# Optimization experiments

Measured on AMD Instinct MI355X. Metric: run time of the kernel, lower is better.

The kernel has to match this reference:

```python
import jax, jax.numpy as jnp
import numpy as np

B = 64; N_PER = 128; N = B * N_PER          # 8192 nodes
E = 32768                                    # edges
X_DIM = 64; EDGE_DIM = 16; D = 512
RING_SIZE = 6; RINGS_PER = 8; R = B * RINGS_PER  # 512 rings
NH_RING = 2; NH_MOL = 4; DFF = 4 * D
GAT_LAYERS = 6; NEG_SLOPE = 0.2


def _ln(x, g, b, eps=1e-5):
    mu = jnp.mean(x, axis=-1, keepdims=True)
    var = jnp.mean((x - mu) ** 2, axis=-1, keepdims=True)
    return (x - mu) * jax.lax.rsqrt(var + eps) * g + b


def _seg_softmax(s, seg, n):
    m = jax.ops.segment_max(s, seg, num_segments=n)
    e = jnp.exp(s - m[seg])
    z = jax.ops.segment_sum(e, seg, num_segments=n)
    return e / z[seg]


def _mha(x, w, b, nh):
    Bq, S, Dm = x.shape
    dh = Dm // nh
    q = (x @ w[0] + b[0]).reshape(Bq, S, nh, dh)
    k = (x @ w[1] + b[1]).reshape(Bq, S, nh, dh)
    v = (x @ w[2] + b[2]).reshape(Bq, S, nh, dh)
    att = jax.nn.softmax(jnp.einsum('bqhd,bkhd->bhqk', q, k) / np.float32(np.sqrt(dh)), axis=-1)
    o = jnp.einsum('bhqk,bkhd->bqhd', att, v).reshape(Bq, S, Dm)
    return o @ w[3] + b[3]


def _encoder(x, aw, ab, w1, b1, w2, b2, lns, nh):
    # post-LN transformer encoder block (1 layer)
    y = _ln(x + _mha(x, aw, ab, nh), lns[0, 0], lns[0, 1])
    h = jnp.maximum(y @ w1 + b1, 0.0) @ w2 + b2
    return _ln(y + h, lns[1, 0], lns[1, 1])


def setup_inputs() -> dict:
    key = jax.random.key(0)
    ks = jax.random.split(key, 24)
    f32 = jnp.float32
    def p(i, shape, s=0.02):
        return jax.random.normal(ks[i], shape, f32) * s
    ln2 = jnp.stack([jnp.stack([jnp.ones((D,), f32), jnp.zeros((D,), f32)])] * 2)  # [2,2,D]
    return {
        'x': jax.random.normal(ks[0], (N, X_DIM), f32),
        'edge_attr': jax.random.normal(ks[1], (E, EDGE_DIM), f32),
        'edge_index': jax.random.randint(ks[2], (2, E), 0, N, jnp.int32),
        'rings_node_index': jax.random.randint(ks[3], (R * RING_SIZE,), 0, N, jnp.int32),
        'rings_node_nums': jnp.full((R,), RING_SIZE, jnp.int32),
        'mol_rings_nums': jnp.full((B,), RINGS_PER, jnp.int32),
        'batch': jnp.repeat(jnp.arange(B, dtype=jnp.int32), N_PER),
        'ptr': jnp.arange(B + 1, dtype=jnp.int32) * N_PER,
        'x_proj_w': p(4, (X_DIM, D)), 'x_proj_b': jnp.zeros((D,), f32),
        'e_proj_w': p(5, (EDGE_DIM, D)), 'e_proj_b': jnp.zeros((D,), f32),
        'gat_wl': p(6, (GAT_LAYERS, D, D)), 'gat_bl': jnp.zeros((GAT_LAYERS, D), f32),
        'gat_wr': p(7, (GAT_LAYERS, D, D)), 'gat_br': jnp.zeros((GAT_LAYERS, D), f32),
        'gat_we': p(8, (GAT_LAYERS, D, D)),
        'gat_att': p(9, (GAT_LAYERS, D)),
        'gat_bias': jnp.zeros((GAT_LAYERS, D), f32),
        'gat_ln': jnp.stack([jnp.ones((GAT_LAYERS - 1, D), f32), jnp.zeros((GAT_LAYERS - 1, D), f32)], axis=1),
        'ring_attn_w': p(10, (4, D, D)), 'ring_attn_b': jnp.zeros((4, D), f32),
        'ring_w1': p(11, (D, DFF)), 'ring_b1': jnp.zeros((DFF,), f32),
        'ring_w2': p(12, (DFF, D)), 'ring_b2': jnp.zeros((D,), f32),
        'ring_ln': ln2,
        'mol_attn_w': p(13, (4, D, D)), 'mol_attn_b': jnp.zeros((4, D), f32),
        'mol_w1': p(14, (D, DFF)), 'mol_b1': jnp.zeros((DFF,), f32),
        'mol_w2': p(15, (DFF, D)), 'mol_b2': jnp.zeros((D,), f32),
        'mol_ln': ln2,
        'cls_tok': p(16, (1, D), 1.0), 'ring_tok': p(17, (1, D), 1.0), 'end_tok': p(18, (1, D), 1.0),
    }


def reference(x, edge_attr, edge_index, rings_node_index, rings_node_nums,
              mol_rings_nums, batch, ptr,
              x_proj_w, x_proj_b, e_proj_w, e_proj_b,
              gat_wl, gat_bl, gat_wr, gat_br, gat_we, gat_att, gat_bias, gat_ln,
              ring_attn_w, ring_attn_b, ring_w1, ring_b1, ring_w2, ring_b2, ring_ln,
              mol_attn_w, mol_attn_b, mol_w1, mol_b1, mol_w2, mol_b2, mol_ln,
              cls_tok, ring_tok, end_tok):
    # 1) input projections
    h = x @ x_proj_w + x_proj_b                   # [N, D]
    e = edge_attr @ e_proj_w + e_proj_b           # [E, D]
    src, dst = edge_index[0], edge_index[1]
    # self-loops with mean incoming edge attr (PyG fill_value='mean')
    deg = jax.ops.segment_sum(jnp.ones((E,), h.dtype), dst, num_segments=N)
    loop_e = jax.ops.segment_sum(e, dst, num_segments=N) / jnp.maximum(deg, 1.0)[:, None]
    loops = jnp.arange(N, dtype=src.dtype)
    src_e = jnp.concatenate([src, loops])
    dst_e = jnp.concatenate([dst, loops])
    e_all = jnp.concatenate([e, loop_e], axis=0)  # [E+N, D]
    # 2) 6-layer GATv2 (heads=1), LayerNorm+ReLU between layers
    for l in range(GAT_LAYERS):
        xl = h @ gat_wl[l] + gat_bl[l]
        xr = h @ gat_wr[l] + gat_br[l]
        m = jax.nn.leaky_relu(xl[src_e] + xr[dst_e] + e_all @ gat_we[l], NEG_SLOPE)
        a = _seg_softmax(m @ gat_att[l], dst_e, N)
        out = jax.ops.segment_sum(a[:, None] * xl[src_e], dst_e, num_segments=N) + gat_bias[l]
        if l < GAT_LAYERS - 1:
            out = jnp.maximum(_ln(out, gat_ln[l, 0], gat_ln[l, 1]), 0.0)
        h = out
    # 3) rings attention: gather ring atoms, encode, per-channel abs-argmax gather
    t = h[rings_node_index].reshape(R, RING_SIZE, D)
    t = _encoder(t, ring_attn_w, ring_attn_b, ring_w1, ring_b1, ring_w2, ring_b2, ring_ln, NH_RING)
    idx = jnp.argmax(jnp.abs(t), axis=1)                         # [R, D]
    rings_vec = jnp.take_along_axis(t, idx[:, None, :], axis=1)[:, 0, :]  # [R, D]
    # 4) split/pad per molecule (uniform sizes -> reshape) and assemble sequence
    X = h.reshape(B, N_PER, D)
    Xr = rings_vec.reshape(B, RINGS_PER, D)
    seq = jnp.concatenate([
        jnp.broadcast_to(cls_tok[None], (B, 1, D)), X,
        jnp.broadcast_to(ring_tok[None], (B, 1, D)), Xr,
        jnp.broadcast_to(end_tok[None], (B, 1, D))], axis=1)     # [B, 139, D]
    seq = _encoder(seq, mol_attn_w, mol_attn_b, mol_w1, mol_b1, mol_w2, mol_b2, mol_ln, NH_MOL)
    not_padded_X = jnp.ones((B, N_PER), dtype=bool)
    not_padded_Xr = jnp.ones((B, RINGS_PER), dtype=bool)
    return seq, not_padded_X, not_padded_Xr
```

## Files before the change

kernel.cpp:

```cpp
#include <hip/hip_runtime.h>
#include <math.h>


#define DEV __device__ __forceinline__

constexpr int NN   = 8192;
constexpr int EE   = 32768;
constexpr int ENL  = EE + NN;
constexpr int D    = 512;
constexpr int RGS  = 512;
constexpr int RS   = 6;
constexpr int BMOL = 64;
constexpr int SEQS = 139;
constexpr int NSEQ = BMOL * SEQS;
constexpr int MHAT = 8960;
constexpr int DFF  = 2048;

typedef short bf8 __attribute__((ext_vector_type(8)));
typedef float f32x4 __attribute__((ext_vector_type(4)));
typedef _Float16 half2_t __attribute__((ext_vector_type(2)));
typedef _Float16 half8_t __attribute__((ext_vector_type(8)));

#ifdef __has_builtin
#if __has_builtin(__builtin_amdgcn_fdot2)
#define HAS_FDOT2 1
#endif
#endif
#ifndef HAS_FDOT2
#define HAS_FDOT2 0
#endif

DEV float wsum(float v) {
    for (int o = 32; o > 0; o >>= 1) v += __shfl_xor(v, o, 64);
    return v;
}
DEV float wmax(float v) {
    for (int o = 32; o > 0; o >>= 1) v = fmaxf(v, __shfl_xor(v, o, 64));
    return v;
}
DEV unsigned short f2bf(float x) {
    unsigned u = __float_as_uint(x);
    u += 0x7FFFu + ((u >> 16) & 1u);
    return (unsigned short)(u >> 16);
}
DEV float bf2f(unsigned short h) { return __uint_as_float((unsigned)h << 16); }

DEV float dot8(half8_t a, half8_t b, float acc) {
#if HAS_FDOT2
    acc = __builtin_amdgcn_fdot2(__builtin_shufflevector(a, a, 0, 1),
                                 __builtin_shufflevector(b, b, 0, 1), acc, false);
    acc = __builtin_amdgcn_fdot2(__builtin_shufflevector(a, a, 2, 3),
                                 __builtin_shufflevector(b, b, 2, 3), acc, false);
    acc = __builtin_amdgcn_fdot2(__builtin_shufflevector(a, a, 4, 5),
                                 __builtin_shufflevector(b, b, 4, 5), acc, false);
    acc = __builtin_amdgcn_fdot2(__builtin_shufflevector(a, a, 6, 7),
                                 __builtin_shufflevector(b, b, 6, 7), acc, false);
#else
#pragma unroll
    for (int i = 0; i < 8; ++i) acc += (float)a[i] * (float)b[i];
#endif
    return acc;
}

struct GB {
    const float* A;
    const float* B0; const float* B1; const float* B2;
    const float* bias0; const float* bias1; const float* bias2;
    float* C0; float* C1; float* C2;
    int M, N, K, flags, kparts, ksz;
    long long cstride;
};

__global__ __launch_bounds__(256) void gemm_f32b(GB g) {
    __shared__ float As[16][132];
    __shared__ float Bs[16][128];
    const int z = blockIdx.z;
    const int bb = z / g.kparts, kp = z % g.kparts;
    const float* B = bb == 0 ? g.B0 : (bb == 1 ? g.B1 : g.B2);
    const float* bias = bb == 0 ? g.bias0 : (bb == 1 ? g.bias1 : g.bias2);
    float* C = (bb == 0 ? g.C0 : (bb == 1 ? g.C1 : g.C2)) + (size_t)kp * g.cstride;
    const int M = g.M, N = g.N;

    const int tid = threadIdx.x;
    const int wv = tid >> 6, ln = tid & 63;
    const int mg = ((ln >> 3) & 7) | ((wv & 1) << 3);
    const int ng = (ln & 7) | ((wv >> 1) << 3);
    const int m0 = blockIdx.x * 128, n0 = blockIdx.y * 128;

    const int a_row = tid >> 2;
    const int a_kg  = tid & 3;
    const int b_row = tid >> 5;
    const int b_cg  = tid & 31;

    float acc[8][8] = {};
    const int kbeg = kp * g.ksz, kend = kbeg + g.ksz;
    for (int k0 = kbeg; k0 < kend; k0 += 16) {
#pragma unroll
        for (int i = 0; i < 2; ++i) {
            int r = a_row + i * 64;
            int gr = m0 + r; if (gr >= M) gr = M - 1;
            float4 av = *(const float4*)&g.A[(size_t)gr * g.K + k0 + a_kg * 4];
            As[a_kg * 4 + 0][r] = av.x;
            As[a_kg * 4 + 1][r] = av.y;
            As[a_kg * 4 + 2][r] = av.z;
            As[a_kg * 4 + 3][r] = av.w;
        }
#pragma unroll
        for (int i = 0; i < 2; ++i) {
            int r = b_row + i * 8;
            float4 bv = *(const float4*)&B[(size_t)(k0 + r) * N + n0 + b_cg * 4];
            *(float4*)&Bs[r][b_cg * 4] = bv;
        }
        __syncthreads();
#pragma unroll
        for (int k = 0; k < 16; ++k) {
            float a0[8], b0[8];
            *(float4*)&a0[0] = *(const float4*)&As[k][mg * 8];
            *(float4*)&a0[4] = *(const float4*)&As[k][mg * 8 + 4];
            *(float4*)&b0[0] = *(const float4*)&Bs[k][ng * 8];
            *(float4*)&b0[4] = *(const float4*)&Bs[k][ng * 8 + 4];
#pragma unroll
            for (int i = 0; i < 8; ++i)
#pragma unroll
                for (int j = 0; j < 8; ++j) acc[i][j] += a0[i] * b0[j];
        }
        __syncthreads();
    }
#pragma unroll
    for (int i = 0; i < 8; ++i) {
        int gr = m0 + mg * 8 + i;
        if (gr >= M) break;
        float* cp = &C[(size_t)gr * N + n0 + ng * 8];
        float o[8];
#pragma unroll
        for (int j = 0; j < 8; ++j) o[j] = acc[i][j];
        if ((g.flags & 1) && g.kparts == 1) {
            const float* bp = bias + n0 + ng * 8;
#pragma unroll
            for (int j = 0; j < 8; ++j) o[j] += bp[j];
        }
        if (g.flags & 2) {
#pragma unroll
            for (int j = 0; j < 8; ++j) o[j] = fmaxf(o[j], 0.f);
        }
        *(float4*)&cp[0] = make_float4(o[0], o[1], o[2], o[3]);
        *(float4*)&cp[4] = make_float4(o[4], o[5], o[6], o[7]);
    }
}

__global__ __launch_bounds__(256) void gemm_split3(
    const unsigned short* __restrict__ Ah, const unsigned short* __restrict__ Al,
    const unsigned short* __restrict__ Bh, const unsigned short* __restrict__ Bl,
    const float* __restrict__ bias, float* __restrict__ C,
    unsigned short* __restrict__ Ch, unsigned short* __restrict__ Cl,
    int N, int K, int flags, long long bstride, long long cstride, int biasstride)
{
    __shared__ unsigned short sA[2][128][40];
    __shared__ unsigned short sB[2][128][40];
    const int z = blockIdx.z;
    Bh += (size_t)z * bstride; Bl += (size_t)z * bstride;
    if (bias) bias += (size_t)z * biasstride;
    if (C) C += (size_t)z * cstride;
    const int tid = threadIdx.x;
    const int wv = tid >> 6, lane = tid & 63;
    const int m0 = blockIdx.x * 128, n0 = blockIdx.y * 128;
    const int srow = tid >> 2, sc8 = (tid & 3) * 8;
    const int mw = (wv & 1) * 64, nw = (wv >> 1) * 64;
    const int fr = lane & 15, fq = lane >> 4;
    const int ko = fq * 8;

    f32x4 acc[4][4];
    f32x4 zero = {0.f, 0.f, 0.f, 0.f};
#pragma unroll
    for (int i = 0; i < 4; ++i)
#pragma unroll
        for (int j = 0; j < 4; ++j) acc[i][j] = zero;

    for (int k0 = 0; k0 < K; k0 += 32) {
#pragma unroll
        for (int h = 0; h < 2; ++h) {
            int r = srow + h * 64;
            *(bf8*)&sA[0][r][sc8] = *(const bf8*)&Ah[(size_t)(m0 + r) * K + k0 + sc8];
            *(bf8*)&sA[1][r][sc8] = *(const bf8*)&Al[(size_t)(m0 + r) * K + k0 + sc8];
            *(bf8*)&sB[0][r][sc8] = *(const bf8*)&Bh[(size_t)(n0 + r) * K + k0 + sc8];
            *(bf8*)&sB[1][r][sc8] = *(const bf8*)&Bl[(size_t)(n0 + r) * K + k0 + sc8];
        }
        __syncthreads();
        bf8 ah[4], al[4], bh[4], bl[4];
#pragma unroll
        for (int t = 0; t < 4; ++t) {
            ah[t] = *(const bf8*)&sA[0][mw + t * 16 + fr][ko];
            al[t] = *(const bf8*)&sA[1][mw + t * 16 + fr][ko];
            bh[t] = *(const bf8*)&sB[0][nw + t * 16 + fr][ko];
            bl[t] = *(const bf8*)&sB[1][nw + t * 16 + fr][ko];
        }
#pragma unroll
        for (int i = 0; i < 4; ++i)
#pragma unroll
            for (int j = 0; j < 4; ++j) {
                acc[i][j] = __builtin_amdgcn_mfma_f32_16x16x32_bf16(ah[i], bh[j], acc[i][j], 0, 0, 0);
                acc[i][j] = __builtin_amdgcn_mfma_f32_16x16x32_bf16(ah[i], bl[j], acc[i][j], 0, 0, 0);
                acc[i][j] = __builtin_amdgcn_mfma_f32_16x16x32_bf16(al[i], bh[j], acc[i][j], 0, 0, 0);
            }
        __syncthreads();
    }
#pragma unroll
    for (int i = 0; i < 4; ++i)
#pragma unroll
        for (int j = 0; j < 4; ++j) {
            int col = n0 + nw + j * 16 + fr;
#pragma unroll
            for (int r = 0; r < 4; ++r) {
                int row = m0 + mw + i * 16 + fq * 4 + r;
                float o = acc[i][j][r];
                if (flags & 1) o += bias[col];
                if (flags & 2) o = fmaxf(o, 0.f);
                size_t idx = (size_t)row * N + col;
                if (flags & 4) {
                    unsigned short hb_ = f2bf(o);
                    Ch[idx] = hb_;
                    Cl[idx] = f2bf(o - bf2f(hb_));
                } else {
                    C[idx] = o;
                }
            }
        }
}

__global__ void asplit4(const float* __restrict__ src, unsigned short* __restrict__ hh,
                        unsigned short* __restrict__ ll, int n4) {
    int i = blockIdx.x * 256 + threadIdx.x;
    if (i >= n4) return;
    float4 v = ((const float4*)src)[i];
    ushort4 h, l;
    h.x = f2bf(v.x); l.x = f2bf(v.x - bf2f(h.x));
    h.y = f2bf(v.y); l.y = f2bf(v.y - bf2f(h.y));
    h.z = f2bf(v.z); l.z = f2bf(v.z - bf2f(h.z));
    h.w = f2bf(v.w); l.w = f2bf(v.w - bf2f(h.w));
    ((ushort4*)hh)[i] = h;
    ((ushort4*)ll)[i] = l;
}

__global__ void wsplitT(const float* __restrict__ w, unsigned short* __restrict__ bh,
                        unsigned short* __restrict__ bl, int K, int N) {
    int i = blockIdx.x * 256 + threadIdx.x;
    if (i >= K * N) return;
    int k = i / N, n = i - k * N;
    float x = w[i];
    unsigned short h = f2bf(x);
    unsigned short l = f2bf(x - bf2f(h));
    bh[(size_t)n * K + k] = h;
    bl[(size_t)n * K + k] = l;
}

__global__ __launch_bounds__(256) void ln_rows(
    const float* __restrict__ x, const float* __restrict__ res,
    const float* __restrict__ bias, const float* __restrict__ g,
    const float* __restrict__ be, float* __restrict__ out, int rows, int flags,
    int parts)
{
    int r = blockIdx.x * 4 + (threadIdx.x >> 6);
    if (r >= rows) return;
    int lane = threadIdx.x & 63;
    size_t base = (size_t)r * D;
    size_t pstride = (size_t)rows * D;
    float v[8];
#pragma unroll
    for (int i = 0; i < 8; ++i) {
        int d = lane + i * 64;
        float t = x[base + d];
        for (int p = 1; p < parts; ++p) t += x[p * pstride + base + d];
        if (res)  t += res[base + d];
        if (bias) t += bias[d];
        v[i] = t;
    }
    if (flags & 2) {
        float s = 0;
#pragma unroll
        for (int i = 0; i < 8; ++i) s += v[i];
        float mu = wsum(s) * (1.f / 512.f);
        float q = 0;
#pragma unroll
        for (int i = 0; i < 8; ++i) { float d0 = v[i] - mu; q += d0 * d0; }
        float inv = rsqrtf(wsum(q) * (1.f / 512.f) + 1e-5f);
#pragma unroll
        for (int i = 0; i < 8; ++i) {
            int d = lane + i * 64;
            float o = (v[i] - mu) * inv * g[d] + be[d];
            if (flags & 1) o = fmaxf(o, 0.f);
            out[base + d] = o;
        }
    } else {
#pragma unroll
        for (int i = 0; i < 8; ++i) {
            int d = lane + i * 64;
            float o = v[i];
            if (flags & 1) o = fmaxf(o, 0.f);
            out[base + d] = o;
        }
    }
}

__global__ void fill_f32(float* p, float v, int n) {
    int i = blockIdx.x * 256 + threadIdx.x;
    if (i < n) p[i] = v;
}

__global__ void deg_int(const int* __restrict__ ei, int* __restrict__ degi) {
    int e = blockIdx.x * 256 + threadIdx.x;
    if (e >= EE) return;
    atomicAdd(&degi[ei[EE + e]], 1);
}

__global__ __launch_bounds__(256) void scan_deg(const int* __restrict__ degi,
                                                int* __restrict__ off) {
    __shared__ int ps[256];
    int tid = threadIdx.x;
    int base = tid * 32;
    int loc[32];
    int s = 0;
#pragma unroll
    for (int i = 0; i < 32; ++i) { loc[i] = s; s += degi[base + i]; }
    ps[tid] = s;
    __syncthreads();
    for (int o = 1; o < 256; o <<= 1) {
        int v = (tid >= o) ? ps[tid - o] : 0;
        __syncthreads();
        ps[tid] += v;
        __syncthreads();
    }
    int pre = (tid == 0) ? 0 : ps[tid - 1];
#pragma unroll
    for (int i = 0; i < 32; ++i) off[base + i] = pre + loc[i];
    if (tid == 255) off[8192] = ps[255];
}

__global__ void csr_fill(const int* __restrict__ ei, int* __restrict__ cnt,
                         const int* __restrict__ off, int* __restrict__ adj) {
    int e = blockIdx.x * 256 + threadIdx.x;
    if (e >= EE) return;
    int dn = ei[EE + e];
    int p = atomicAdd(&cnt[dn], 1);
    adj[off[dn] + p] = e;
}

__global__ void eagg_acc(const float* __restrict__ eattr, const int* __restrict__ ei,
                         float* __restrict__ agg) {
    int id = blockIdx.x * 256 + threadIdx.x;
    if (id >= EE * 16) return;
    int e = id >> 4, c = id & 15;
    atomicAdd(&agg[(size_t)ei[EE + e] * 16 + c], eattr[id]);
}

__global__ void ein_build(const float* __restrict__ eattr, const float* __restrict__ agg,
                          const int* __restrict__ degi, float* __restrict__ ein) {
    int r = blockIdx.x * 256 + threadIdx.x;
    if (r >= ENL) return;
    float* o = &ein[(size_t)r * 17];
    if (r < EE) {
        const float* a = &eattr[(size_t)r * 16];
#pragma unroll
        for (int k = 0; k < 16; ++k) o[k] = a[k];
        o[16] = 1.f;
    } else {
        int n = r - EE;
        int dg = degi[n];
        float inv = 1.f / (float)(dg > 1 ? dg : 1);
        const float* a = &agg[(size_t)n * 16];
#pragma unroll
        for (int k = 0; k < 16; ++k) o[k] = a[k] * inv;
        o[16] = dg > 0 ? 1.f : 0.f;
    }
}

__global__ __launch_bounds__(256) void we17_build(
    const float* __restrict__ epw, const float* __restrict__ epb,
    const float* __restrict__ we_all, float* __restrict__ we17_all) {
    int j = blockIdx.x * 256 + threadIdx.x;
    int kk = blockIdx.y, l = blockIdx.z;
    const float* we = we_all + (size_t)l * D * D;
    float* we17 = we17_all + (size_t)l * 17 * D;
    float acc[17];
#pragma unroll
    for (int i = 0; i < 17; ++i) acc[i] = 0.f;
    for (int k = kk * 128; k < kk * 128 + 128; ++k) {
        float wkj = we[(size_t)k * 512 + j];
#pragma unroll
        for (int i = 0; i < 16; ++i) acc[i] += epw[(size_t)i * 512 + k] * wkj;
        acc[16] += epb[k] * wkj;
    }
#pragma unroll
    for (int i = 0; i < 17; ++i) atomicAdd(&we17[(size_t)i * 512 + j], acc[i]);
}

__global__ __launch_bounds__(256) void gat_node(
    const float* __restrict__ xl, const float* __restrict__ xr,
    const float* __restrict__ ein, const float* __restrict__ we17,
    const int* __restrict__ off, const int* __restrict__ adj,
    const int* __restrict__ ei, const float* __restrict__ att,
    float* __restrict__ out)
{
    __shared__ float we[17][512];
    __shared__ float sc[4][88];
    int tid = threadIdx.x;
    for (int i = tid; i < 17 * 512; i += 256) we[i >> 9][i & 511] = we17[i];
    __syncthreads();
    int wv = tid >> 6, lane = tid & 63;
    int n = blockIdx.x * 4 + wv;
    float xr8[8], att8[8];
#pragma unroll
    for (int i = 0; i < 8; ++i) {
        int d = lane + i * 64;
        xr8[i] = xr[(size_t)n * D + d];
        att8[i] = att[d];
    }
    int o0 = off[n];
    int deg = off[n + 1] - o0;
    if (deg > 80) deg = 80;
    for (int j = 0; j <= deg; ++j) {
        int er, s;
        if (j < deg) { int e = adj[o0 + j]; er = e; s = ei[e]; }
        else         { er = EE + n; s = n; }
        const float* ep = &ein[(size_t)er * 17];
        float e17[17];
#pragma unroll
        for (int k = 0; k < 17; ++k) e17[k] = ep[k];
        float a = 0;
#pragma unroll
        for (int i = 0; i < 8; ++i) {
            int d = lane + i * 64;
            float m = xl[(size_t)s * D + d] + xr8[i];
#pragma unroll
            for (int k = 0; k < 17; ++k) m += e17[k] * we[k][d];
            m = m > 0.f ? m : 0.2f * m;
            a += att8[i] * m;
        }
        a = wsum(a);
        if (lane == 0) sc[wv][j] = a;
    }
    __syncthreads();
    float mx = -1e30f;
    for (int j = 0; j <= deg; ++j) mx = fmaxf(mx, sc[wv][j]);
    float z = 0;
    for (int j = 0; j <= deg; ++j) z += expf(sc[wv][j] - mx);
    float acc[8] = {};
    for (int j = 0; j <= deg; ++j) {
        int s = (j < deg) ? ei[adj[o0 + j]] : n;
        float w = expf(sc[wv][j] - mx);
#pragma unroll
        for (int i = 0; i < 8; ++i) acc[i] += w * xl[(size_t)s * D + lane + i * 64];
    }
    float inv = 1.f / z;
#pragma unroll
    for (int i = 0; i < 8; ++i) out[(size_t)n * D + lane + i * 64] = acc[i] * inv;
}

__global__ void gather_rows(const float* __restrict__ src, const int* __restrict__ idx,
                            float* __restrict__ dst, int nrows) {
    int i = blockIdx.x * 256 + threadIdx.x;
    int r = i >> 9;
    if (r >= nrows) return;
    dst[i] = src[(size_t)idx[r] * D + (i & 511)];
}

__global__ __launch_bounds__(256) void ring_attn(
    const float* __restrict__ q, const float* __restrict__ k,
    const float* __restrict__ v, float* __restrict__ o)
{
    int rh = blockIdx.x, r = rh >> 1, hh = rh & 1;
    __shared__ float qs[RS * 256], ks[RS * 256], vs[RS * 256];
    __shared__ float scs[36], pr[36];
    int tid = threadIdx.x;
    size_t base = (size_t)r * RS * D + hh * 256;
    for (int i = tid; i < RS * 256; i += 256) {
        int si = i >> 8, d = i & 255;
        size_t g = base + (size_t)si * D + d;
        qs[i] = q[g]; ks[i] = k[g]; vs[i] = v[g];
    }
    __syncthreads();
    if (tid < 36) {
        int i = tid / 6, j = tid % 6;
        float a = 0;
        for (int d = 0; d < 256; ++d) a += qs[i * 256 + d] * ks[j * 256 + d];
        scs[tid] = a * (1.f / 16.f);
    }
    __syncthreads();
    if (tid < 6) {
        float mx = -1e30f;
        for (int j = 0; j < 6; ++j) mx = fmaxf(mx, scs[tid * 6 + j]);
        float p[6], s = 0;
        for (int j = 0; j < 6; ++j) { p[j] = expf(scs[tid * 6 + j] - mx); s += p[j]; }
        for (int j = 0; j < 6; ++j) pr[tid * 6 + j] = p[j] / s;
    }
    __syncthreads();
    for (int i = tid; i < RS * 256; i += 256) {
        int si = i >> 8, d = i & 255;
        float a = 0;
        for (int j = 0; j < 6; ++j) a += pr[si * 6 + j] * vs[j * 256 + d];
        o[base + (size_t)si * D + d] = a;
    }
}

constexpr int ATT_K_H  = SEQS * 128;
constexpr int ATT_V_ROW = 152;
constexpr int ATT_V_H  = 128 * ATT_V_ROW;
constexpr int ATT_PS_ROW = 144;
constexpr int ATT_PS_H = 8 * ATT_PS_ROW;
constexpr int ATT_SMEM = (ATT_K_H + ATT_V_H + ATT_PS_H) * 2 + 8 * 64 * 4;

__global__ __launch_bounds__(256) void mol_attn3(
    const float* __restrict__ q, const float* __restrict__ k,
    const float* __restrict__ v, float* __restrict__ o)
{
    extern __shared__ char smem[];
    _Float16* Ksh = (_Float16*)smem;
    _Float16* Vt  = Ksh + ATT_K_H;
    _Float16* ps  = Vt + ATT_V_H;
    half2_t*  qs  = (half2_t*)(ps + ATT_PS_H);
    const int tid = threadIdx.x, wv = tid >> 6, lane = tid & 63;
    const int b = blockIdx.x >> 2, hh = blockIdx.x & 3;
    const size_t hb = (size_t)b * SEQS * D + hh * 128;

    for (int i = tid; i < SEQS * 32; i += 256) {
        int j = i >> 5, d4 = i & 31;
        float4 kv = *(const float4*)&k[hb + (size_t)j * D + d4 * 4];
        int off = j * 128 + (((d4 >> 1) ^ (j & 7)) << 3) + ((d4 & 1) << 2);
        *(half2_t*)(Ksh + off)     = half2_t{(_Float16)kv.x, (_Float16)kv.y};
        *(half2_t*)(Ksh + off + 2) = half2_t{(_Float16)kv.z, (_Float16)kv.w};
    }
    for (int i = tid; i < SEQS * 32; i += 256) {
        int j = i >> 5, d4 = i & 31;
        float4 vv = *(const float4*)&v[hb + (size_t)j * D + d4 * 4];
        Vt[(d4 * 4 + 0) * ATT_V_ROW + j] = (_Float16)vv.x;
        Vt[(d4 * 4 + 1) * ATT_V_ROW + j] = (_Float16)vv.y;
        Vt[(d4 * 4 + 2) * ATT_V_ROW + j] = (_Float16)vv.z;
        Vt[(d4 * 4 + 3) * ATT_V_ROW + j] = (_Float16)vv.w;
    }
    for (int i = tid; i < 128 * 5; i += 256) {
        int d = i / 5, jt = SEQS + i % 5;
        Vt[d * ATT_V_ROW + jt] = (_Float16)0.f;
    }
    __syncthreads();

    const float scale = 0.08838834764831845f;
    for (int t = 0; t < 18; ++t) {
        int p = wv + 4 * t;
        if (p >= 70) continue;
        int q0 = 2 * p, q1 = 2 * p + 1;
        bool h1 = q1 < SEQS;
        {
            float2 f0 = *(const float2*)&q[hb + (size_t)q0 * D + lane * 2];
            qs[(wv * 2 + 0) * 64 + lane] = half2_t{(_Float16)f0.x, (_Float16)f0.y};
            if (h1) {
                float2 f1 = *(const float2*)&q[hb + (size_t)q1 * D + lane * 2];
                qs[(wv * 2 + 1) * 64 + lane] = half2_t{(_Float16)f1.x, (_Float16)f1.y};
            }
        }
        float s0[3], s1[3];
#pragma unroll
        for (int jj = 0; jj < 3; ++jj) { s0[jj] = -1e30f; s1[jj] = -1e30f; }
#pragma unroll
        for (int jj = 0; jj < 3; ++jj) {
            int j = lane + jj * 64;
            if (j < SEQS) {
                float a0 = 0, a1 = 0;
                const int jb = j * 128, jx = j & 7;
#pragma unroll
                for (int c = 0; c < 16; ++c) {
                    half8_t kk = *(const half8_t*)(Ksh + jb + ((c ^ jx) << 3));
                    half8_t q0v = *(const half8_t*)(qs + (wv * 2 + 0) * 64 + c * 4);
                    a0 = dot8(kk, q0v, a0);
                    if (h1) {
                        half8_t q1v = *(const half8_t*)(qs + (wv * 2 + 1) * 64 + c * 4);
                        a1 = dot8(kk, q1v, a1);
                    }
                }
                s0[jj] = a0 * scale; s1[jj] = a1 * scale;
            }
        }
        {
            float m0 = wmax(fmaxf(fmaxf(s0[0], s0[1]), s0[2]));
            float z0 = 0; float e0[3];
#pragma unroll
            for (int jj = 0; jj < 3; ++jj) {
                int j = lane + jj * 64;
                e0[jj] = (j < SEQS) ? expf(s0[jj] - m0) : 0.f;
                z0 += e0[jj];
            }
            z0 = wsum(z0); float inv0 = 1.f / z0;
#pragma unroll
            for (int jj = 0; jj < 3; ++jj) {
                int j = lane + jj * 64;
                if (j < ATT_PS_ROW) ps[(wv * 2 + 0) * ATT_PS_ROW + j] = (_Float16)(e0[jj] * inv0);
            }
        }
        if (h1) {
            float m1 = wmax(fmaxf(fmaxf(s1[0], s1[1]), s1[2]));
            float z1 = 0; float e1[3];
#pragma unroll
            for (int jj = 0; jj < 3; ++jj) {
                int j = lane + jj * 64;
                e1[jj] = (j < SEQS) ? expf(s1[jj] - m1) : 0.f;
                z1 += e1[jj];
            }
            z1 = wsum(z1); float inv1 = 1.f / z1;
#pragma unroll
            for (int jj = 0; jj < 3; ++jj) {
                int j = lane + jj * 64;
                if (j < ATT_PS_ROW) ps[(wv * 2 + 1) * ATT_PS_ROW + j] = (_Float16)(e1[jj] * inv1);
            }
        }
        float o00 = 0, o01 = 0, o10 = 0, o11 = 0;
#pragma unroll
        for (int c8 = 0; c8 < 18; ++c8) {
            half8_t va = *(const half8_t*)(Vt + lane * ATT_V_ROW + c8 * 8);
            half8_t vb = *(const half8_t*)(Vt + (lane + 64) * ATT_V_ROW + c8 * 8);
            half8_t p0 = *(const half8_t*)(ps + (wv * 2 + 0) * ATT_PS_ROW + c8 * 8);
            o00 = dot8(va, p0, o00);
            o01 = dot8(vb, p0, o01);
            if (h1) {
                half8_t p1 = *(const half8_t*)(ps + (wv * 2 + 1) * ATT_PS_ROW + c8 * 8);
                o10 = dot8(va, p1, o10);
                o11 = dot8(vb, p1, o11);
            }
        }
        o[hb + (size_t)q0 * D + lane]      = o00;
        o[hb + (size_t)q0 * D + lane + 64] = o01;
        if (h1) {
            o[hb + (size_t)q1 * D + lane]      = o10;
            o[hb + (size_t)q1 * D + lane + 64] = o11;
        }
    }
}

__global__ void ring_pick(const float* __restrict__ t, float* __restrict__ rv) {
    int i = blockIdx.x * 256 + threadIdx.x;
    if (i >= RGS * D) return;
    int r = i >> 9, d = i & 511;
    const float* p = &t[(size_t)r * RS * D + d];
    float best = p[0], ba = fabsf(best);
#pragma unroll
    for (int s = 1; s < RS; ++s) {
        float x = p[(size_t)s * D];
        float ax = fabsf(x);
        if (ax > ba) { ba = ax; best = x; }
    }
    rv[i] = best;
}

__global__ void assemble(const float* __restrict__ h, const float* __restrict__ rv,
                         const float* __restrict__ cls, const float* __restrict__ ringt,
                         const float* __restrict__ endt, float* __restrict__ seq) {
    int i = blockIdx.x * 256 + threadIdx.x;
    if (i >= NSEQ * D) return;
    int row = i >> 9, d = i & 511;
    int b = row / SEQS, p = row % SEQS;
    float val;
    if (p == 0)        val = cls[d];
    else if (p <= 128) val = h[((size_t)b * 128 + (p - 1)) * D + d];
    else if (p == 129) val = ringt[d];
    else if (p <= 137) val = rv[((size_t)b * 8 + (p - 130)) * D + d];
    else               val = endt[d];
    seq[i] = val;
}

extern "C" void kernel_launch(void* const* d_in, const int* in_sizes, int n_in,
                              void* d_out, int out_size, void* d_ws, size_t ws_size,
                              hipStream_t stream) {
    (void)in_sizes; (void)n_in; (void)out_size; (void)ws_size;

    const float* x          = (const float*)d_in[0];
    const float* edge_attr  = (const float*)d_in[1];
    const int*   ei         = (const int*)  d_in[2];
    const int*   rings_idx  = (const int*)  d_in[3];
    const float* x_proj_w   = (const float*)d_in[8];
    const float* x_proj_b   = (const float*)d_in[9];
    const float* e_proj_w   = (const float*)d_in[10];
    const float* e_proj_b   = (const float*)d_in[11];
    const float* gat_wl     = (const float*)d_in[12];
    const float* gat_bl     = (const float*)d_in[13];
    const float* gat_wr     = (const float*)d_in[14];
    const float* gat_br     = (const float*)d_in[15];
    const float* gat_we     = (const float*)d_in[16];
    const float* gat_att    = (const float*)d_in[17];
    const float* gat_bias   = (const float*)d_in[18];
    const float* gat_ln     = (const float*)d_in[19];
    const float* ring_attn_w= (const float*)d_in[20];
    const float* ring_attn_b= (const float*)d_in[21];
    const float* ring_w1    = (const float*)d_in[22];
    const float* ring_b1    = (const float*)d_in[23];
    const float* ring_w2    = (const float*)d_in[24];
    const float* ring_b2    = (const float*)d_in[25];
    const float* ring_ln    = (const float*)d_in[26];
    const float* mol_attn_w = (const float*)d_in[27];
    const float* mol_attn_b = (const float*)d_in[28];
    const float* mol_w1     = (const float*)d_in[29];
    const float* mol_b1     = (const float*)d_in[30];
    const float* mol_w2     = (const float*)d_in[31];
    const float* mol_b2     = (const float*)d_in[32];
    const float* mol_ln     = (const float*)d_in[33];
    const float* cls_tok    = (const float*)d_in[34];
    const float* ring_tok   = (const float*)d_in[35];
    const float* end_tok    = (const float*)d_in[36];

    constexpr size_t MB = 1024 * 1024;
    char* wsb = (char*)d_ws;
#define WSF(off) ((float*)(wsb + (size_t)(off)))
#define WSI(off) ((int*)(wsb + (size_t)(off)))
#define WSU(off) ((unsigned short*)(wsb + (size_t)(off)))

    float* H    = WSF(0);
    float* XL   = WSF(16 * MB);
    float* XR   = WSF(32 * MB);
    float* HN   = WSF(48 * MB);
    float* EIN  = WSF(64 * MB);
    float* WE17 = WSF(67 * MB);
    float* AGG  = WSF(68 * MB);
    int*   DEGI = WSI(68 * MB + 512 * 1024);
    int*   OFF  = WSI(68 * MB + 576 * 1024);
    int*   CNT  = WSI(68 * MB + 640 * 1024);
    int*   ADJ  = WSI(68 * MB + 704 * 1024);
    float* RVEC = WSF(70 * MB);

    float* T    = WSF(71 * MB);
    float* RQ   = WSF(77 * MB);
    float* RK   = WSF(83 * MB);
    float* RV   = WSF(89 * MB);
    float* RO   = WSF(95 * MB);
    float* OP   = WSF(101 * MB);
    float* RY   = WSF(113 * MB);
    float* RFF  = WSF(119 * MB);
    float* W2P  = WSF(143 * MB);
    float* RT2  = WSF(167 * MB);

    float* SEQ  = WSF(71 * MB);
    float* MQKV = WSF(89 * MB);
    float* MO   = WSF(142 * MB);
    unsigned short* ACTh = WSU(161 * MB);
    unsigned short* ACTl = WSU(170 * MB);
    unsigned short* WQKVh = WSU(179 * MB);
    unsigned short* WQKVl = WSU(181 * MB);
    unsigned short* WOh  = WSU(183 * MB);
    unsigned short* WOl  = WSU(183 * MB + 512 * 1024);
    unsigned short* W1h  = WSU(184 * MB);
    unsigned short* W1l  = WSU(186 * MB);
    unsigned short* W2h  = WSU(188 * MB);
    unsigned short* W2l  = WSU(190 * MB);
    float* MTMP = WSF(89 * MB);
    float* MY   = WSF(107 * MB);
    unsigned short* MFFh = WSU(125 * MB);
    unsigned short* MFFl = WSU(16 * MB);
    float* MT2  = WSF(71 * MB);

    dim3 blk(256);
    auto gemm1 = [&](const float* A, const float* B, const float* bias, float* C,
                     int M, int Nc, int K, int flags) {
        GB g{A, B, nullptr, nullptr, bias, nullptr, nullptr, C, nullptr, nullptr,
             M, Nc, K, flags, 1, K, 0};
        gemm_f32b<<<dim3(M / 128, Nc / 128, 1), blk, 0, stream>>>(g);
    };

    hipMemsetAsync(DEGI, 0, NN * 4, stream);
    hipMemsetAsync(CNT, 0, NN * 4, stream);
    hipMemsetAsync(AGG, 0, (size_t)NN * 16 * 4, stream);
    hipMemsetAsync(WE17, 0, (size_t)6 * 17 * D * 4, stream);
    deg_int<<<EE / 256, blk, 0, stream>>>(ei, DEGI);
    scan_deg<<<1, blk, 0, stream>>>(DEGI, OFF);
    csr_fill<<<EE / 256, blk, 0, stream>>>(ei, CNT, OFF, ADJ);
    eagg_acc<<<EE * 16 / 256, blk, 0, stream>>>(edge_attr, ei, AGG);
    ein_build<<<ENL / 256, blk, 0, stream>>>(edge_attr, AGG, DEGI, EIN);
    we17_build<<<dim3(2, 4, 6), blk, 0, stream>>>(e_proj_w, e_proj_b, gat_we, WE17);

    gemm1(x, x_proj_w, x_proj_b, H, NN, D, 64, 1);

    for (int l = 0; l < 6; ++l) {
        GB g{H, gat_wl + (size_t)l * D * D, gat_wr + (size_t)l * D * D, nullptr,
             gat_bl + l * D, gat_br + l * D, nullptr,
             XL, XR, nullptr, NN, D, D, 1, 1, D, 0};
        gemm_f32b<<<dim3(NN / 128, D / 128, 2), blk, 0, stream>>>(g);
        gat_node<<<NN / 4, blk, 0, stream>>>(XL, XR, EIN, WE17 + (size_t)l * 17 * D,
                                             OFF, ADJ, ei, gat_att + l * D, HN);
        if (l < 5) {
            ln_rows<<<NN / 4, blk, 0, stream>>>(HN, nullptr, gat_bias + l * D,
                gat_ln + (size_t)l * 2 * D, gat_ln + (size_t)l * 2 * D + D, H, NN, 3, 1);
        } else {
            ln_rows<<<NN / 4, blk, 0, stream>>>(HN, nullptr, gat_bias + l * D,
                nullptr, nullptr, H, NN, 0, 1);
        }
    }

    const int RROWS = RGS * RS;
    gather_rows<<<RROWS * D / 256, blk, 0, stream>>>(H, rings_idx, T, RROWS);
    {
        GB g{T, ring_attn_w + 0 * D * D, ring_attn_w + 1 * D * D, ring_attn_w + 2 * D * D,
             ring_attn_b + 0 * D, ring_attn_b + 1 * D, ring_attn_b + 2 * D,
             RQ, RK, RV, RROWS, D, D, 1, 1, D, 0};
        gemm_f32b<<<dim3(RROWS / 128, D / 128, 3), blk, 0, stream>>>(g);
    }
    ring_attn<<<RGS * 2, blk, 0, stream>>>(RQ, RK, RV, RO);
    {
        GB g{RO, ring_attn_w + 3 * D * D, nullptr, nullptr, nullptr, nullptr, nullptr,
             OP, nullptr, nullptr, RROWS, D, D, 0, 2, 256, (long long)RROWS * D};
        gemm_f32b<<<dim3(RROWS / 128, D / 128, 2), blk, 0, stream>>>(g);
    }
    ln_rows<<<RROWS / 4, blk, 0, stream>>>(OP, T, ring_attn_b + 3 * D,
                                           ring_ln, ring_ln + D, RY, RROWS, 2, 2);
    gemm1(RY, ring_w1, ring_b1, RFF, RROWS, DFF, D, 3);
    {
        GB g{RFF, ring_w2, nullptr, nullptr, nullptr, nullptr, nullptr,
             W2P, nullptr, nullptr, RROWS, D, DFF, 0, 4, 512, (long long)RROWS * D};
        gemm_f32b<<<dim3(RROWS / 128, D / 128, 4), blk, 0, stream>>>(g);
    }
    ln_rows<<<RROWS / 4, blk, 0, stream>>>(W2P, RY, ring_b2,
                                           ring_ln + 2 * D, ring_ln + 3 * D, RT2, RROWS, 2, 4);
    ring_pick<<<RGS * D / 256, blk, 0, stream>>>(RT2, RVEC);

    assemble<<<(NSEQ * D) / 256, blk, 0, stream>>>(H, RVEC, cls_tok, ring_tok, end_tok, SEQ);
    for (int z = 0; z < 3; ++z)
        wsplitT<<<(D * D + 255) / 256, blk, 0, stream>>>(
            mol_attn_w + (size_t)z * D * D, WQKVh + (size_t)z * D * D, WQKVl + (size_t)z * D * D, D, D);
    wsplitT<<<(D * D + 255) / 256, blk, 0, stream>>>(mol_attn_w + 3 * (size_t)D * D, WOh, WOl, D, D);
    wsplitT<<<(D * DFF + 255) / 256, blk, 0, stream>>>(mol_w1, W1h, W1l, D, DFF);
    wsplitT<<<(DFF * D + 255) / 256, blk, 0, stream>>>(mol_w2, W2h, W2l, DFF, D);

    const int N4_512 = MHAT * D / 4;
    float* MQ = MQKV;
    float* MK = MQKV + (size_t)MHAT * D;
    float* MV = MQKV + 2 * (size_t)MHAT * D;
    asplit4<<<(N4_512 + 255) / 256, blk, 0, stream>>>(SEQ, ACTh, ACTl, N4_512);
    gemm_split3<<<dim3(MHAT / 128, D / 128, 3), blk, 0, stream>>>(
        ACTh, ACTl, WQKVh, WQKVl, mol_attn_b, MQKV, nullptr, nullptr,
        D, D, 1, (long long)D * D, (long long)MHAT * D, D);

    hipFuncSetAttribute(reinterpret_cast<const void*>(mol_attn3),
                        hipFuncAttributeMaxDynamicSharedMemorySize, ATT_SMEM);
    mol_attn3<<<BMOL * 4, blk, ATT_SMEM, stream>>>(MQ, MK, MV, MO);

    asplit4<<<(N4_512 + 255) / 256, blk, 0, stream>>>(MO, ACTh, ACTl, N4_512);
    gemm_split3<<<dim3(MHAT / 128, D / 128, 1), blk, 0, stream>>>(
        ACTh, ACTl, WOh, WOl, mol_attn_b + 3 * D, MTMP, nullptr, nullptr, D, D, 1, 0, 0, 0);
    ln_rows<<<(NSEQ + 3) / 4, blk, 0, stream>>>(MTMP, SEQ, nullptr,
                                                mol_ln, mol_ln + D, MY, NSEQ, 2, 1);
    asplit4<<<(N4_512 + 255) / 256, blk, 0, stream>>>(MY, ACTh, ACTl, N4_512);
    gemm_split3<<<dim3(MHAT / 128, DFF / 128, 1), blk, 0, stream>>>(
        ACTh, ACTl, W1h, W1l, mol_b1, nullptr, MFFh, MFFl, DFF, D, 1 | 2 | 4, 0, 0, 0);
    gemm_split3<<<dim3(MHAT / 128, D / 128, 1), blk, 0, stream>>>(
        MFFh, MFFl, W2h, W2l, mol_b2, MT2, nullptr, nullptr, D, DFF, 1, 0, 0, 0);

    float* outf = (float*)d_out;
    ln_rows<<<(NSEQ + 3) / 4, blk, 0, stream>>>(MT2, MY, nullptr,
                                                mol_ln + 2 * D, mol_ln + 3 * D, outf, NSEQ, 2, 1);
    fill_f32<<<(BMOL * 128 + BMOL * 8 + 255) / 256, blk, 0, stream>>>(
        outf + (size_t)NSEQ * D, 1.0f, BMOL * 128 + BMOL * 8);
}
```

Baseline: 2.318 ms.

## Split-K GEMMs with atomic accumulation, swap grid axes, fuse QKV into one GEMM

The fp32 GEMM kernel gains an atomic-accumulate mode: GAT and ring projections run split-K into zeroed buffers, with the bias added only by the first K-part. ReLU is moved from the W1 epilogue into the W2 A-load so split-K stays correct. Grid axes are swapped so N tiles vary fastest, aiming for better reuse of A rows in cache. The molecule QKV projection becomes one GEMM with N=1536 and interleaved output rows read by attention through a row stride. In exchange it adds memsets and atomic traffic, and it assumes the split-3 weights are laid out contiguously so a single N=1536 GEMM is valid.

Result: slower. 5.386 ms (+132.4%).

```diff
diff --git a/kernel.cpp b/kernel.cpp
--- a/kernel.cpp
+++ b/kernel.cpp
@@ -75,17 +75,18 @@
     __shared__ float As[16][132];
     __shared__ float Bs[16][128];
     const int z = blockIdx.z;
-    const int bb = z / g.kparts, kp = z % g.kparts;
+    const int bb = z / g.kparts, kp = z - bb * g.kparts;
     const float* B = bb == 0 ? g.B0 : (bb == 1 ? g.B1 : g.B2);
     const float* bias = bb == 0 ? g.bias0 : (bb == 1 ? g.bias1 : g.bias2);
-    float* C = (bb == 0 ? g.C0 : (bb == 1 ? g.C1 : g.C2)) + (size_t)kp * g.cstride;
+    float* C = (bb == 0 ? g.C0 : (bb == 1 ? g.C1 : g.C2));
+    if (!(g.flags & 4)) C += (size_t)kp * g.cstride;
     const int M = g.M, N = g.N;
 
     const int tid = threadIdx.x;
     const int wv = tid >> 6, ln = tid & 63;
     const int mg = ((ln >> 3) & 7) | ((wv & 1) << 3);
     const int ng = (ln & 7) | ((wv >> 1) << 3);
-    const int m0 = blockIdx.x * 128, n0 = blockIdx.y * 128;
+    const int m0 = blockIdx.y * 128, n0 = blockIdx.x * 128;
 
     const int a_row = tid >> 2;
     const int a_kg  = tid & 3;
@@ -100,6 +101,10 @@
             int r = a_row + i * 64;
             int gr = m0 + r; if (gr >= M) gr = M - 1;
             float4 av = *(const float4*)&g.A[(size_t)gr * g.K + k0 + a_kg * 4];
+            if (g.flags & 8) {
+                av.x = fmaxf(av.x, 0.f); av.y = fmaxf(av.y, 0.f);
+                av.z = fmaxf(av.z, 0.f); av.w = fmaxf(av.w, 0.f);
+            }
             As[a_kg * 4 + 0][r] = av.x;
             As[a_kg * 4 + 1][r] = av.y;
             As[a_kg * 4 + 2][r] = av.z;
@@ -134,17 +139,22 @@
         float o[8];
 #pragma unroll
         for (int j = 0; j < 8; ++j) o[j] = acc[i][j];
-        if ((g.flags & 1) && g.kparts == 1) {
+        if ((g.flags & 1) && kp == 0) {
             const float* bp = bias + n0 + ng * 8;
 #pragma unroll
             for (int j = 0; j < 8; ++j) o[j] += bp[j];
         }
-        if (g.flags & 2) {
+        if ((g.flags & 2) && g.kparts == 1) {
 #pragma unroll
             for (int j = 0; j < 8; ++j) o[j] = fmaxf(o[j], 0.f);
         }
-        *(float4*)&cp[0] = make_float4(o[0], o[1], o[2], o[3]);
-        *(float4*)&cp[4] = make_float4(o[4], o[5], o[6], o[7]);
+        if (g.flags & 4) {
+#pragma unroll
+            for (int j = 0; j < 8; ++j) atomicAdd(&cp[j], o[j]);
+        } else {
+            *(float4*)&cp[0] = make_float4(o[0], o[1], o[2], o[3]);
+            *(float4*)&cp[4] = make_float4(o[4], o[5], o[6], o[7]);
+        }
     }
 }
 
@@ -153,17 +163,13 @@
     const unsigned short* __restrict__ Bh, const unsigned short* __restrict__ Bl,
     const float* __restrict__ bias, float* __restrict__ C,
     unsigned short* __restrict__ Ch, unsigned short* __restrict__ Cl,
-    int N, int K, int flags, long long bstride, long long cstride, int biasstride)
+    int N, int K, int flags)
 {
     __shared__ unsigned short sA[2][128][40];
     __shared__ unsigned short sB[2][128][40];
-    const int z = blockIdx.z;
-    Bh += (size_t)z * bstride; Bl += (size_t)z * bstride;
-    if (bias) bias += (size_t)z * biasstride;
-    if (C) C += (size_t)z * cstride;
     const int tid = threadIdx.x;
     const int wv = tid >> 6, lane = tid & 63;
-    const int m0 = blockIdx.x * 128, n0 = blockIdx.y * 128;
+    const int m0 = blockIdx.y * 128, n0 = blockIdx.x * 128;
     const int srow = tid >> 2, sc8 = (tid & 3) * 8;
     const int mw = (wv & 1) * 64, nw = (wv >> 1) * 64;
     const int fr = lane & 15, fq = lane >> 4;
@@ -510,7 +516,7 @@
 
 __global__ __launch_bounds__(256) void mol_attn3(
     const float* __restrict__ q, const float* __restrict__ k,
-    const float* __restrict__ v, float* __restrict__ o)
+    const float* __restrict__ v, float* __restrict__ o, int rs)
 {
     extern __shared__ char smem[];
     _Float16* Ksh = (_Float16*)smem;
@@ -519,18 +525,19 @@
     half2_t*  qs  = (half2_t*)(ps + ATT_PS_H);
     const int tid = threadIdx.x, wv = tid >> 6, lane = tid & 63;
     const int b = blockIdx.x >> 2, hh = blockIdx.x & 3;
-    const size_t hb = (size_t)b * SEQS * D + hh * 128;
+    const size_t hb = (size_t)b * SEQS * rs + hh * 128;
+    const size_t ob = (size_t)b * SEQS * D + hh * 128;
 
     for (int i = tid; i < SEQS * 32; i += 256) {
         int j = i >> 5, d4 = i & 31;
-        float4 kv = *(const float4*)&k[hb + (size_t)j * D + d4 * 4];
+        float4 kv = *(const float4*)&k[hb + (size_t)j * rs + d4 * 4];
         int off = j * 128 + (((d4 >> 1) ^ (j & 7)) << 3) + ((d4 & 1) << 2);
         *(half2_t*)(Ksh + off)     = half2_t{(_Float16)kv.x, (_Float16)kv.y};
         *(half2_t*)(Ksh + off + 2) = half2_t{(_Float16)kv.z, (_Float16)kv.w};
     }
     for (int i = tid; i < SEQS * 32; i += 256) {
         int j = i >> 5, d4 = i & 31;
-        float4 vv = *(const float4*)&v[hb + (size_t)j * D + d4 * 4];
+        float4 vv = *(const float4*)&v[hb + (size_t)j * rs + d4 * 4];
         Vt[(d4 * 4 + 0) * ATT_V_ROW + j] = (_Float16)vv.x;
         Vt[(d4 * 4 + 1) * ATT_V_ROW + j] = (_Float16)vv.y;
         Vt[(d4 * 4 + 2) * ATT_V_ROW + j] = (_Float16)vv.z;
@@ -549,10 +556,10 @@
         int q0 = 2 * p, q1 = 2 * p + 1;
         bool h1 = q1 < SEQS;
         {
-            float2 f0 = *(const float2*)&q[hb + (size_t)q0 * D + lane * 2];
+            float2 f0 = *(const float2*)&q[hb + (size_t)q0 * rs + lane * 2];
             qs[(wv * 2 + 0) * 64 + lane] = half2_t{(_Float16)f0.x, (_Float16)f0.y};
             if (h1) {
-                float2 f1 = *(const float2*)&q[hb + (size_t)q1 * D + lane * 2];
+                float2 f1 = *(const float2*)&q[hb + (size_t)q1 * rs + lane * 2];
                 qs[(wv * 2 + 1) * 64 + lane] = half2_t{(_Float16)f1.x, (_Float16)f1.y};
             }
         }
@@ -624,11 +631,11 @@
                 o11 = dot8(vb, p1, o11);
             }
         }
-        o[hb + (size_t)q0 * D + lane]      = o00;
-        o[hb + (size_t)q0 * D + lane + 64] = o01;
+        o[ob + (size_t)q0 * D + lane]      = o00;
+        o[ob + (size_t)q0 * D + lane + 64] = o01;
         if (h1) {
-            o[hb + (size_t)q1 * D + lane]      = o10;
-            o[hb + (size_t)q1 * D + lane + 64] = o11;
+            o[ob + (size_t)q1 * D + lane]      = o10;
+            o[ob + (size_t)q1 * D + lane + 64] = o11;
         }
     }
 }
@@ -753,12 +760,6 @@
     float* MT2  = WSF(71 * MB);
 
     dim3 blk(256);
-    auto gemm1 = [&](const float* A, const float* B, const float* bias, float* C,
-                     int M, int Nc, int K, int flags) {
-        GB g{A, B, nullptr, nullptr, bias, nullptr, nullptr, C, nullptr, nullptr,
-             M, Nc, K, flags, 1, K, 0};
-        gemm_f32b<<<dim3(M / 128, Nc / 128, 1), blk, 0, stream>>>(g);
-    };
 
     hipMemsetAsync(DEGI, 0, NN * 4, stream);
     hipMemsetAsync(CNT, 0, NN * 4, stream);
@@ -771,13 +772,19 @@
     ein_build<<<ENL / 256, blk, 0, stream>>>(edge_attr, AGG, DEGI, EIN);
     we17_build<<<dim3(2, 4, 6), blk, 0, stream>>>(e_proj_w, e_proj_b, gat_we, WE17);
 
-    gemm1(x, x_proj_w, x_proj_b, H, NN, D, 64, 1);
+    {
+        GB g{x, x_proj_w, nullptr, nullptr, x_proj_b, nullptr, nullptr,
+             H, nullptr, nullptr, NN, D, 64, 1, 1, 64, 0};
+        gemm_f32b<<<dim3(D / 128, NN / 128, 1), blk, 0, stream>>>(g);
+    }
 
     for (int l = 0; l < 6; ++l) {
+        hipMemsetAsync(XL, 0, (size_t)NN * D * 4, stream);
+        hipMemsetAsync(XR, 0, (size_t)NN * D * 4, stream);
         GB g{H, gat_wl + (size_t)l * D * D, gat_wr + (size_t)l * D * D, nullptr,
              gat_bl + l * D, gat_br + l * D, nullptr,
-             XL, XR, nullptr, NN, D, D, 1, 1, D, 0};
-        gemm_f32b<<<dim3(NN / 128, D / 128, 2), blk, 0, stream>>>(g);
+             XL, XR, nullptr, NN, D, D, 1 | 4, 2, 256, 0};
+        gemm_f32b<<<dim3(D / 128, NN / 128, 4), blk, 0, stream>>>(g);
         gat_node<<<NN / 4, blk, 0, stream>>>(XL, XR, EIN, WE17 + (size_t)l * 17 * D,
                                              OFF, ADJ, ei, gat_att + l * D, HN);
         if (l < 5) {
@@ -791,25 +798,31 @@
 
     const int RROWS = RGS * RS;
     gather_rows<<<RROWS * D / 256, blk, 0, stream>>>(H, rings_idx, T, RROWS);
+    hipMemsetAsync(RQ, 0, (size_t)3 * RROWS * D * 4, stream);
     {
         GB g{T, ring_attn_w + 0 * D * D, ring_attn_w + 1 * D * D, ring_attn_w + 2 * D * D,
              ring_attn_b + 0 * D, ring_attn_b + 1 * D, ring_attn_b + 2 * D,
-             RQ, RK, RV, RROWS, D, D, 1, 1, D, 0};
-        gemm_f32b<<<dim3(RROWS / 128, D / 128, 3), blk, 0, stream>>>(g);
+             RQ, RK, RV, RROWS, D, D, 1 | 4, 2, 256, 0};
+        gemm_f32b<<<dim3(D / 128, RROWS / 128, 6), blk, 0, stream>>>(g);
     }
     ring_attn<<<RGS * 2, blk, 0, stream>>>(RQ, RK, RV, RO);
     {
         GB g{RO, ring_attn_w + 3 * D * D, nullptr, nullptr, nullptr, nullptr, nullptr,
              OP, nullptr, nullptr, RROWS, D, D, 0, 2, 256, (long long)RROWS * D};
-        gemm_f32b<<<dim3(RROWS / 128, D / 128, 2), blk, 0, stream>>>(g);
+        gemm_f32b<<<dim3(D / 128, RROWS / 128, 2), blk, 0, stream>>>(g);
     }
     ln_rows<<<RROWS / 4, blk, 0, stream>>>(OP, T, ring_attn_b + 3 * D,
                                            ring_ln, ring_ln + D, RY, RROWS, 2, 2);
-    gemm1(RY, ring_w1, ring_b1, RFF, RROWS, DFF, D, 3);
+    hipMemsetAsync(RFF, 0, (size_t)RROWS * DFF * 4, stream);
+    {
+        GB g{RY, ring_w1, nullptr, nullptr, ring_b1, nullptr, nullptr,
+             RFF, nullptr, nullptr, RROWS, DFF, D, 1 | 4, 2, 256, 0};
+        gemm_f32b<<<dim3(DFF / 128, RROWS / 128, 2), blk, 0, stream>>>(g);
+    }
     {
         GB g{RFF, ring_w2, nullptr, nullptr, nullptr, nullptr, nullptr,
-             W2P, nullptr, nullptr, RROWS, D, DFF, 0, 4, 512, (long long)RROWS * D};
-        gemm_f32b<<<dim3(RROWS / 128, D / 128, 4), blk, 0, stream>>>(g);
+             W2P, nullptr, nullptr, RROWS, D, DFF, 8, 4, 512, (long long)RROWS * D};
+        gemm_f32b<<<dim3(D / 128, RROWS / 128, 4), blk, 0, stream>>>(g);
     }
     ln_rows<<<RROWS / 4, blk, 0, stream>>>(W2P, RY, ring_b2,
                                            ring_ln + 2 * D, ring_ln + 3 * D, RT2, RROWS, 2, 4);
@@ -825,27 +838,26 @@
 
     const int N4_512 = MHAT * D / 4;
     float* MQ = MQKV;
-    float* MK = MQKV + (size_t)MHAT * D;
-    float* MV = MQKV + 2 * (size_t)MHAT * D;
+    float* MK = MQKV + 512;
+    float* MV = MQKV + 1024;
     asplit4<<<(N4_512 + 255) / 256, blk, 0, stream>>>(SEQ, ACTh, ACTl, N4_512);
-    gemm_split3<<<dim3(MHAT / 128, D / 128, 3), blk, 0, stream>>>(
-        ACTh, ACTl, WQKVh, WQKVl, mol_attn_b, MQKV, nullptr, nullptr,
-        D, D, 1, (long long)D * D, (long long)MHAT * D, D);
+    gemm_split3<<<dim3(1536 / 128, MHAT / 128), blk, 0, stream>>>(
+        ACTh, ACTl, WQKVh, WQKVl, mol_attn_b, MQKV, nullptr, nullptr, 1536, D, 1);
 
     hipFuncSetAttribute(reinterpret_cast<const void*>(mol_attn3),
                         hipFuncAttributeMaxDynamicSharedMemorySize, ATT_SMEM);
-    mol_attn3<<<BMOL * 4, blk, ATT_SMEM, stream>>>(MQ, MK, MV, MO);
+    mol_attn3<<<BMOL * 4, blk, ATT_SMEM, stream>>>(MQ, MK, MV, MO, 1536);
 
     asplit4<<<(N4_512 + 255) / 256, blk, 0, stream>>>(MO, ACTh, ACTl, N4_512);
-    gemm_split3<<<dim3(MHAT / 128, D / 128, 1), blk, 0, stream>>>(
-        ACTh, ACTl, WOh, WOl, mol_attn_b + 3 * D, MTMP, nullptr, nullptr, D, D, 1, 0, 0, 0);
+    gemm_split3<<<dim3(D / 128, MHAT / 128), blk, 0, stream>>>(
+        ACTh, ACTl, WOh, WOl, mol_attn_b + 3 * D, MTMP, nullptr, nullptr, D, D, 1);
     ln_rows<<<(NSEQ + 3) / 4, blk, 0, stream>>>(MTMP, SEQ, nullptr,
                                                 mol_ln, mol_ln + D, MY, NSEQ, 2, 1);
     asplit4<<<(N4_512 + 255) / 256, blk, 0, stream>>>(MY, ACTh, ACTl, N4_512);
-    gemm_split3<<<dim3(MHAT / 128, DFF / 128, 1), blk, 0, stream>>>(
-        ACTh, ACTl, W1h, W1l, mol_b1, nullptr, MFFh, MFFl, DFF, D, 1 | 2 | 4, 0, 0, 0);
-    gemm_split3<<<dim3(MHAT / 128, D / 128, 1), blk, 0, stream>>>(
-        MFFh, MFFl, W2h, W2l, mol_b2, MT2, nullptr, nullptr, D, DFF, 1, 0, 0, 0);
+    gemm_split3<<<dim3(DFF / 128, MHAT / 128), blk, 0, stream>>>(
+        ACTh, ACTl, W1h, W1l, mol_b1, nullptr, MFFh, MFFl, DFF, D, 1 | 2 | 4);
+    gemm_split3<<<dim3(D / 128, MHAT / 128), blk, 0, stream>>>(
+        MFFh, MFFl, W2h, W2l, mol_b2, MT2, nullptr, nullptr, D, DFF, 1);
 
     float* outf = (float*)d_out;
     ln_rows<<<(NSEQ + 3) / 4, blk, 0, stream>>>(MT2, MY, nullptr,
```
